# Performance work log

Hardware: AMD Instinct MI355X
Metric: run time of the kernel (lower is better)

Reference implementation:

```python
import jax, jax.numpy as jnp
import numpy as np

U, T, K, Q, H = 4096, 200, 64, 10000, 128
STD_THETA = 1.0


def setup_inputs() -> dict:
    key = jax.random.key(0)
    ks = jax.random.split(key, 12)
    q_id = jax.random.randint(ks[0], (U, T), 0, Q, dtype=jnp.int32)
    resp = jax.random.randint(ks[1], (U, T), 0, 2, dtype=jnp.int32)
    # one KC per question so the per-timestep masked_select size is constant (= U)
    kc_of_q = jax.random.randint(ks[2], (Q,), 0, K)
    kmap = jax.nn.one_hot(kc_of_q, K, dtype=jnp.float32) > 0.5  # (Q, K) bool, one-hot
    mask = jnp.ones((U, T), dtype=bool)
    diff_mu = jax.random.normal(ks[3], (Q,), dtype=jnp.float32)
    disc_mu = jax.random.normal(ks[4], (Q,), dtype=jnp.float32)
    xav = lambda k, fi, fo: jax.random.normal(k, (fi, fo), dtype=jnp.float32) * (2.0 / (fi + fo)) ** 0.5
    W1 = xav(ks[5], 3, H)
    W2 = xav(ks[6], H, H)
    W3 = xav(ks[7], H, 2)
    b1 = jnp.zeros((H,), jnp.float32)
    b2 = jnp.zeros((H,), jnp.float32)
    b3 = jnp.zeros((2,), jnp.float32)
    return dict(mask=mask, q_id=q_id, kmap=kmap, resp=resp,
                diff_mu=diff_mu, disc_mu=disc_mu,
                W1=W1, b1=b1, W2=W2, b2=b2, W3=W3, b3=b3)


def reference(mask, q_id, kmap, resp, diff_mu, disc_mu, W1, b1, W2, b2, W3, b3):
    gelu = lambda x: jax.nn.gelu(x, approximate=False)  # torch nn.GELU default = exact erf
    nu = q_id.shape[0]
    td = diff_mu[q_id]                      # (U, T) trial difficulty
    ts = disc_mu[q_id]                      # (U, T) trial discrimination
    x = jnp.stack([td, ts, resp.astype(jnp.float32)], axis=-1)  # (U, T, 3)
    h = gelu(gelu(x @ W1 + b1) @ W2 + b2)
    out = gelu(h @ W3 + b3)                 # (U, T, 2)
    mu = out[..., 0].T                      # (T, U)
    logvar = out[..., 1].T                  # (T, U)
    std = jnp.maximum(jnp.exp(0.5 * logvar), 1e-8)
    r = (STD_THETA / std) ** 2              # (T, U)

    # backward Kalman-style recursion: b_t = 1/(1 + r_t + (1 - b_{t+1})), c_t = b_t*(c_{t+1} + r_t*mu_t)
    def bwd_step(carry, rm):
        b_n, c_n = carry
        r_t, mu_t = rm
        b_t = 1.0 / (1.0 + r_t + (1.0 - b_n))
        c_t = b_t * (c_n + r_t * mu_t)
        return (b_t, c_t), (b_t, c_t)

    init = (jnp.ones((nu,), mu.dtype), jnp.zeros((nu,), mu.dtype))
    _, (b_seq, c_seq) = jax.lax.scan(bwd_step, init, (r, mu), reverse=True)  # (T, U) each

    # forward pass: gather active-KC ability, update, scatter back into per-user KC state
    active_kc = jnp.argmax(kmap[q_id], axis=-1).T  # (T, U) one active KC per trial
    uidx = jnp.arange(nu)

    def fwd_step(curr, bck):
        b_t, c_t, kc_t = bck
        prev = curr[uidx, kc_t]
        mu_t = b_t * prev + c_t
        curr = curr.at[uidx, kc_t].set(mu_t)
        return curr, mu_t

    curr0 = jnp.zeros((nu, kmap.shape[1]), mu.dtype)
    last_ability_kc, ability_T = jax.lax.scan(fwd_step, curr0, (b_seq, c_seq, active_kc))
    ability = ability_T.T                   # (U, T): masked mean over one-hot KC = active KC ability
    trial_logits = ts * (ability - td)      # (U, T)
    return trial_logits, last_ability_kc
```

## Files before the change

### kernel.cpp

```cpp
#include <hip/hip_runtime.h>
#include <math.h>

#define U_ 4096
#define T_ 200
#define K_ 64
#define Q_ 10000
#define H_ 128
#define UPB 8
#define PPB 32

__device__ __forceinline__ float gelu_f(float x) {
  return 0.5f * x * (1.0f + erff(x * 0.70710678118654752440f));
}

__global__ __launch_bounds__(256, 4) void mlp_table_kernel(
    const float* __restrict__ diff_mu, const float* __restrict__ disc_mu,
    const float* __restrict__ W1, const float* __restrict__ b1,
    const float* __restrict__ W2, const float* __restrict__ b2,
    const float* __restrict__ W3, const float* __restrict__ b3,
    const unsigned char* __restrict__ kmap,
    float4* __restrict__ tab4, int* __restrict__ kc_of_q) {
  __shared__ __align__(16) float W2s[64 * H_];
  __shared__ __align__(16) float h1buf[PPB][H_ + 4];

  const int tid = threadIdx.x;
  const int lane = tid & 63, w = tid >> 6;
  const int base = blockIdx.x * PPB;

  if (blockIdx.x < 40) {
    int q = blockIdx.x * 256 + tid;
    if (q < Q_) {
      const unsigned char* km = kmap + (size_t)q * K_;
      int kc = 0;
#pragma unroll
      for (int k = 0; k < K_; ++k)
        if (km[k]) kc = k;
      kc_of_q[q] = kc;
    }
  }

  for (int v = tid; v < PPB * H_; v += 256) {
    int pl = v >> 7, j = v & 127;
    int pg = base + pl, q = pg >> 1;
    float rf = (float)(pg & 1);
    float a = fmaf(diff_mu[q], W1[j], b1[j]);
    a = fmaf(disc_mu[q], W1[H_ + j], a);
    a = fmaf(rf, W1[2 * H_ + j], a);
    h1buf[pl][j] = gelu_f(a);
  }
  for (int v = tid; v < 2048; v += 256)
    ((float4*)W2s)[v] = ((const float4*)W2)[v];
  __syncthreads();

  float a0[8], a1[8];
#pragma unroll
  for (int p = 0; p < 8; ++p) { a0[p] = 0.f; a1[p] = 0.f; }

#pragma clang loop unroll_count(2)
  for (int kq = 0; kq < 64; kq += 4) {
    float2 wv[4];
#pragma unroll
    for (int kk = 0; kk < 4; ++kk)
      wv[kk] = *(const float2*)&W2s[(kq + kk) * H_ + 2 * lane];
#pragma unroll
    for (int p = 0; p < 8; ++p) {
      float4 hv = *(const float4*)&h1buf[w * 8 + p][kq];
      a0[p] = fmaf(wv[0].x, hv.x, a0[p]); a1[p] = fmaf(wv[0].y, hv.x, a1[p]);
      a0[p] = fmaf(wv[1].x, hv.y, a0[p]); a1[p] = fmaf(wv[1].y, hv.y, a1[p]);
      a0[p] = fmaf(wv[2].x, hv.z, a0[p]); a1[p] = fmaf(wv[2].y, hv.z, a1[p]);
      a0[p] = fmaf(wv[3].x, hv.w, a0[p]); a1[p] = fmaf(wv[3].y, hv.w, a1[p]);
    }
  }
  __syncthreads();
  for (int v = tid; v < 2048; v += 256)
    ((float4*)W2s)[v] = ((const float4*)W2)[2048 + v];
  __syncthreads();
#pragma clang loop unroll_count(2)
  for (int kq = 0; kq < 64; kq += 4) {
    float2 wv[4];
#pragma unroll
    for (int kk = 0; kk < 4; ++kk)
      wv[kk] = *(const float2*)&W2s[(kq + kk) * H_ + 2 * lane];
#pragma unroll
    for (int p = 0; p < 8; ++p) {
      float4 hv = *(const float4*)&h1buf[w * 8 + p][64 + kq];
      a0[p] = fmaf(wv[0].x, hv.x, a0[p]); a1[p] = fmaf(wv[0].y, hv.x, a1[p]);
      a0[p] = fmaf(wv[1].x, hv.y, a0[p]); a1[p] = fmaf(wv[1].y, hv.y, a1[p]);
      a0[p] = fmaf(wv[2].x, hv.z, a0[p]); a1[p] = fmaf(wv[2].y, hv.z, a1[p]);
      a0[p] = fmaf(wv[3].x, hv.w, a0[p]); a1[p] = fmaf(wv[3].y, hv.w, a1[p]);
    }
  }

  float2 b2v = *(const float2*)&b2[2 * lane];
  float4 w3v = *(const float4*)&W3[4 * lane];
  float b30 = b3[0], b31 = b3[1];
#pragma unroll
  for (int p = 0; p < 8; ++p) {
    float h2a = gelu_f(a0[p] + b2v.x);
    float h2b = gelu_f(a1[p] + b2v.y);
    float s0 = h2a * w3v.x + h2b * w3v.z;
    float s1 = h2a * w3v.y + h2b * w3v.w;
#pragma unroll
    for (int off = 32; off > 0; off >>= 1) {
      s0 += __shfl_xor(s0, off, 64);
      s1 += __shfl_xor(s1, off, 64);
    }
    if (lane == 0) {
      float mu = gelu_f(s0 + b30);
      float lv = gelu_f(s1 + b31);
      float sd = fmaxf(expf(0.5f * lv), 1e-8f);
      int pg = base + w * 8 + p;
      int q = pg >> 1;
      tab4[pg] = make_float4(1.0f / (sd * sd), mu, disc_mu[q], diff_mu[q]);
    }
  }
}

__global__ __launch_bounds__(512) void scan_kernel(
    const int* __restrict__ q_id, const int* __restrict__ resp,
    const float4* __restrict__ tab4, const int* __restrict__ kc_of_q,
    float* __restrict__ out) {
  __shared__ __align__(16) float4 q4s[T_ * (UPB + 1)];
  __shared__ unsigned char kcs[T_ * UPB];

  const int tid = threadIdx.x;
  const int lane = tid & 63;
  const int ul = tid >> 6;
  const int gu = blockIdx.x * UPB + ul;

  const int* qrow = q_id + (size_t)gu * T_;
  const int* rrow = resp + (size_t)gu * T_;
#pragma unroll
  for (int i = 0; i < 4; ++i) {
    int t = i * 64 + lane;
    if (t < T_) {
      int q = qrow[t];
      int rp = rrow[t];
      q4s[t * (UPB + 1) + ul] = tab4[q * 2 + rp];
      kcs[t * UPB + ul] = (unsigned char)kc_of_q[q];
    }
  }

  float tb[4], tcc[4];
  float b = 1.0f, c = 0.0f;
#pragma unroll 8
  for (int s = 7; s >= 0; --s) {
    int t = 192 + s;
    float2 rm = *(const float2*)&q4s[t * (UPB + 1) + ul];
    float x_ = 2.0f + rm.x - b;
    float ib = __builtin_amdgcn_rcpf(x_);
    ib = ib * (2.0f - x_ * ib);
    b = ib;
    c = b * fmaf(rm.x, rm.y, c);
    bool cap = (lane == s);
    tb[3] = cap ? b : tb[3];
    tcc[3] = cap ? c : tcc[3];
  }
#pragma unroll
  for (int i = 2; i >= 0; --i) {
#pragma unroll 8
    for (int s = 63; s >= 0; --s) {
      int t = i * 64 + s;
      float2 rm = *(const float2*)&q4s[t * (UPB + 1) + ul];
      float x_ = 2.0f + rm.x - b;
      float ib = __builtin_amdgcn_rcpf(x_);
      ib = ib * (2.0f - x_ * ib);
      b = ib;
      c = b * fmaf(rm.x, rm.y, c);
      bool cap = (lane == s);
      tb[i] = cap ? b : tb[i];
      tcc[i] = cap ? c : tcc[i];
    }
  }
#pragma unroll
  for (int i = 0; i < 4; ++i) {
    int t = i * 64 + lane;
    if (t < T_)
      *(float2*)&q4s[t * (UPB + 1) + ul] = make_float2(tb[i], tcc[i]);
  }

  float x = 0.0f;
  float* logits = out + (size_t)gu * T_;
  float* last = out + (size_t)U_ * T_;
#pragma unroll 8
  for (int t = 0; t < T_; ++t) {
    float4 g = q4s[t * (UPB + 1) + ul];
    int kc = (int)kcs[t * UPB + ul];
    float xn = fmaf(g.x, x, g.y);
    bool hit = (lane == kc);
    x = hit ? xn : x;
    if (hit) logits[t] = g.z * (xn - g.w);
  }
  last[(size_t)gu * K_ + lane] = x;
}

extern "C" void kernel_launch(void* const* d_in, const int* in_sizes, int n_in,
                              void* d_out, int out_size, void* d_ws,
                              size_t ws_size, hipStream_t stream) {
  const int* q_id = (const int*)d_in[1];
  const unsigned char* kmap = (const unsigned char*)d_in[2];
  const int* resp = (const int*)d_in[3];
  const float* diff_mu = (const float*)d_in[4];
  const float* disc_mu = (const float*)d_in[5];
  const float* W1 = (const float*)d_in[6];
  const float* b1 = (const float*)d_in[7];
  const float* W2 = (const float*)d_in[8];
  const float* b2 = (const float*)d_in[9];
  const float* W3 = (const float*)d_in[10];
  const float* b3 = (const float*)d_in[11];
  float* out = (float*)d_out;
  char* ws = (char*)d_ws;

  auto align512 = [](size_t x) { return (x + 511) & ~(size_t)511; };
  size_t o = 0;
  float4* tab4 = (float4*)(ws + o);  o = align512(o + (size_t)2 * Q_ * 16);
  int* kc_of_q = (int*)(ws + o);     o = align512(o + (size_t)Q_ * 4);
  (void)ws_size; (void)in_sizes; (void)n_in; (void)out_size;

  mlp_table_kernel<<<Q_ * 2 / PPB, 256, 0, stream>>>(
      diff_mu, disc_mu, W1, b1, W2, b2, W3, b3, kmap, tab4, kc_of_q);
  scan_kernel<<<U_ / UPB, 512, 0, stream>>>(q_id, resp, tab4, kc_of_q, out);
}
```

Before: 142.9 us.

## Pack KC index into table low bits, precombine Kalman terms, stage logits in LDS

The KC lookup is now computed per question with a wavefront ballot over the kmap row and packed into the low 6 bits of the disc_mu float in the table, so the separate kc_of_q array and its gather disappear. The table stores 2+r and r*mu, which removes an add and an FMA from the serial backward recursion. The LDS layout becomes per-user rows, and logits are staged in LDS during the forward pass, then written with coalesced stores instead of scattered single-lane writes. Overwriting the low mantissa bits of disc_mu introduces a small precision error in the logits.

```diff
diff --git a/kernel.cpp b/kernel.cpp
--- a/kernel.cpp
+++ b/kernel.cpp
@@ -19,7 +19,7 @@
     const float* __restrict__ W2, const float* __restrict__ b2,
     const float* __restrict__ W3, const float* __restrict__ b3,
     const unsigned char* __restrict__ kmap,
-    float4* __restrict__ tab4, int* __restrict__ kc_of_q) {
+    float4* __restrict__ tab4) {
   __shared__ __align__(16) float W2s[64 * H_];
   __shared__ __align__(16) float h1buf[PPB][H_ + 4];
 
@@ -27,16 +27,13 @@
   const int lane = tid & 63, w = tid >> 6;
   const int base = blockIdx.x * PPB;
 
-  if (blockIdx.x < 40) {
-    int q = blockIdx.x * 256 + tid;
-    if (q < Q_) {
-      const unsigned char* km = kmap + (size_t)q * K_;
-      int kc = 0;
-#pragma unroll
-      for (int k = 0; k < K_; ++k)
-        if (km[k]) kc = k;
-      kc_of_q[q] = kc;
-    }
+  const int q0 = blockIdx.x * 16 + w * 4;
+  int kcw[4];
+#pragma unroll
+  for (int qi = 0; qi < 4; ++qi) {
+    unsigned char kb = kmap[(size_t)(q0 + qi) * K_ + lane];
+    unsigned long long m = __ballot(kb != 0);
+    kcw[qi] = (m != 0ull) ? (int)__builtin_ctzll(m) : 0;
   }
 
   for (int v = tid; v < PPB * H_; v += 256) {
@@ -109,19 +106,20 @@
       float mu = gelu_f(s0 + b30);
       float lv = gelu_f(s1 + b31);
       float sd = fmaxf(expf(0.5f * lv), 1e-8f);
+      float r = 1.0f / (sd * sd);
       int pg = base + w * 8 + p;
       int q = pg >> 1;
-      tab4[pg] = make_float4(1.0f / (sd * sd), mu, disc_mu[q], diff_mu[q]);
+      int tsb = (__float_as_int(disc_mu[q]) & ~63) | (kcw[p >> 1] & 63);
+      tab4[pg] = make_float4(2.0f + r, r * mu, __int_as_float(tsb),
+                             diff_mu[q]);
     }
   }
 }
 
 __global__ __launch_bounds__(512) void scan_kernel(
     const int* __restrict__ q_id, const int* __restrict__ resp,
-    const float4* __restrict__ tab4, const int* __restrict__ kc_of_q,
-    float* __restrict__ out) {
-  __shared__ __align__(16) float4 q4s[T_ * (UPB + 1)];
-  __shared__ unsigned char kcs[T_ * UPB];
+    const float4* __restrict__ tab4, float* __restrict__ out) {
+  __shared__ __align__(16) float4 q4s[UPB][T_];
 
   const int tid = threadIdx.x;
   const int lane = tid & 63;
@@ -136,22 +134,20 @@
     if (t < T_) {
       int q = qrow[t];
       int rp = rrow[t];
-      q4s[t * (UPB + 1) + ul] = tab4[q * 2 + rp];
-      kcs[t * UPB + ul] = (unsigned char)kc_of_q[q];
-    }
-  }
-
-  float tb[4], tcc[4];
+      q4s[ul][t] = tab4[q * 2 + rp];
+    }
+  }
+
+  float tb[4] = {0.f, 0.f, 0.f, 0.f}, tcc[4] = {0.f, 0.f, 0.f, 0.f};
   float b = 1.0f, c = 0.0f;
 #pragma unroll 8
   for (int s = 7; s >= 0; --s) {
-    int t = 192 + s;
-    float2 rm = *(const float2*)&q4s[t * (UPB + 1) + ul];
-    float x_ = 2.0f + rm.x - b;
+    float2 rm = *(const float2*)&q4s[ul][192 + s];
+    float x_ = rm.x - b;
     float ib = __builtin_amdgcn_rcpf(x_);
     ib = ib * (2.0f - x_ * ib);
     b = ib;
-    c = b * fmaf(rm.x, rm.y, c);
+    c = b * (rm.y + c);
     bool cap = (lane == s);
     tb[3] = cap ? b : tb[3];
     tcc[3] = cap ? c : tcc[3];
@@ -160,13 +156,12 @@
   for (int i = 2; i >= 0; --i) {
 #pragma unroll 8
     for (int s = 63; s >= 0; --s) {
-      int t = i * 64 + s;
-      float2 rm = *(const float2*)&q4s[t * (UPB + 1) + ul];
-      float x_ = 2.0f + rm.x - b;
+      float2 rm = *(const float2*)&q4s[ul][i * 64 + s];
+      float x_ = rm.x - b;
       float ib = __builtin_amdgcn_rcpf(x_);
       ib = ib * (2.0f - x_ * ib);
       b = ib;
-      c = b * fmaf(rm.x, rm.y, c);
+      c = b * (rm.y + c);
       bool cap = (lane == s);
       tb[i] = cap ? b : tb[i];
       tcc[i] = cap ? c : tcc[i];
@@ -175,21 +170,27 @@
 #pragma unroll
   for (int i = 0; i < 4; ++i) {
     int t = i * 64 + lane;
-    if (t < T_)
-      *(float2*)&q4s[t * (UPB + 1) + ul] = make_float2(tb[i], tcc[i]);
+    if (t < T_) *(float2*)&q4s[ul][t] = make_float2(tb[i], tcc[i]);
   }
 
   float x = 0.0f;
-  float* logits = out + (size_t)gu * T_;
-  float* last = out + (size_t)U_ * T_;
+  float* rowf = (float*)&q4s[ul][0];
 #pragma unroll 8
   for (int t = 0; t < T_; ++t) {
-    float4 g = q4s[t * (UPB + 1) + ul];
-    int kc = (int)kcs[t * UPB + ul];
+    float4 g = q4s[ul][t];
+    int kc = __float_as_int(g.z) & 63;
     float xn = fmaf(g.x, x, g.y);
     bool hit = (lane == kc);
     x = hit ? xn : x;
-    if (hit) logits[t] = g.z * (xn - g.w);
+    if (hit) rowf[t * 4 + 1] = g.z * (xn - g.w);
+  }
+
+  float* logits = out + (size_t)gu * T_;
+  float* last = out + (size_t)U_ * T_;
+#pragma unroll
+  for (int i = 0; i < 4; ++i) {
+    int t = i * 64 + lane;
+    if (t < T_) logits[t] = q4s[ul][t].y;
   }
   last[(size_t)gu * K_ + lane] = x;
 }
@@ -211,13 +212,10 @@
   float* out = (float*)d_out;
   char* ws = (char*)d_ws;
 
-  auto align512 = [](size_t x) { return (x + 511) & ~(size_t)511; };
-  size_t o = 0;
-  float4* tab4 = (float4*)(ws + o);  o = align512(o + (size_t)2 * Q_ * 16);
-  int* kc_of_q = (int*)(ws + o);     o = align512(o + (size_t)Q_ * 4);
+  float4* tab4 = (float4*)ws;
   (void)ws_size; (void)in_sizes; (void)n_in; (void)out_size;
 
   mlp_table_kernel<<<Q_ * 2 / PPB, 256, 0, stream>>>(
-      diff_mu, disc_mu, W1, b1, W2, b2, W3, b3, kmap, tab4, kc_of_q);
-  scan_kernel<<<U_ / UPB, 512, 0, stream>>>(q_id, resp, tab4, kc_of_q, out);
-}
+      diff_mu, disc_mu, W1, b1, W2, b2, W3, b3, kmap, tab4);
+  scan_kernel<<<U_ / UPB, 512, 0, stream>>>(q_id, resp, tab4, out);
+}
```

After: 142.8 us. No clear change (-0.1%).
